# Performance work log

Hardware: AMD Instinct MI355X
Metric: run time of the kernel (lower is better)

The kernel has to match this reference:

```python
import jax, jax.numpy as jnp
import numpy as np

B, S, E = 2, 2048, 4096
H, HKV, D = 32, 8, 128          # num_heads, num_kv_heads, head_dim
ROT = 128                        # rotary_emb_dim (full head)
ROPE_BASE = 10000.0


def setup_inputs() -> dict:
    key = jax.random.key(0)
    ks = jax.random.split(key, 9)
    s = lambda fan_in: 1.0 / np.sqrt(fan_in)
    return {
        "x": jax.random.normal(ks[0], (B, S, E), jnp.float32),
        "wq_w": jax.random.normal(ks[1], (E, E), jnp.float32) * s(E),
        "wq_b": jax.random.normal(ks[2], (E,), jnp.float32) * 0.01,
        "wk_w": jax.random.normal(ks[3], (E, HKV * D), jnp.float32) * s(E),
        "wk_b": jax.random.normal(ks[4], (HKV * D,), jnp.float32) * 0.01,
        "wv_w": jax.random.normal(ks[5], (E, HKV * D), jnp.float32) * s(E),
        "wv_b": jax.random.normal(ks[6], (HKV * D,), jnp.float32) * 0.01,
        "wo_w": jax.random.normal(ks[7], (E, E), jnp.float32) * s(E),
        "wo_b": jax.random.normal(ks[8], (E,), jnp.float32) * 0.01,
    }


def _interleave_to_half(t):
    # torch.cat([t[..., ::2], t[..., 1::2]], dim=-1)
    return jnp.concatenate([t[..., 0::2], t[..., 1::2]], axis=-1)


def _apply_rope(t):
    # non-interleaved (rotate-half) rotary on first ROT dims of head_dim
    half = ROT // 2
    inv_freq = 1.0 / (ROPE_BASE ** (jnp.arange(0, ROT, 2, dtype=jnp.float32) / ROT))
    pos = jnp.arange(t.shape[1], dtype=jnp.float32)
    freqs = pos[:, None] * inv_freq[None, :]            # (S, ROT/2)
    cos = jnp.cos(freqs)[None, :, None, :]              # (1,S,1,ROT/2)
    sin = jnp.sin(freqs)[None, :, None, :]
    t1, t2 = t[..., :half], t[..., half:ROT]
    rot = jnp.concatenate([t1 * cos - t2 * sin, t1 * sin + t2 * cos], axis=-1)
    return jnp.concatenate([rot, t[..., ROT:]], axis=-1)


def reference(x, wq_w, wq_b, wk_w, wk_b, wv_w, wv_b, wo_w, wo_b):
    b, s, _ = x.shape
    q = (x @ wq_w + wq_b).reshape(b, s, H, D)           # bshd
    k = (x @ wk_w + wk_b).reshape(b, s, HKV, D)
    v = (x @ wv_w + wv_b).reshape(b, s, HKV, D)
    # inline even/odd interleave (rot_embed_HF_impl=False path)
    q = _apply_rope(_interleave_to_half(q))
    k = _apply_rope(_interleave_to_half(k))
    # GQA: replicate kv heads
    rep = H // HKV
    k = jnp.repeat(k, rep, axis=2)                      # (b,s,H,D)
    v = jnp.repeat(v, rep, axis=2)
    scale = 1.0 / jnp.sqrt(jnp.asarray(D, x.dtype))
    scores = jnp.einsum("bqhd,bkhd->bhqk", q, k) * scale
    causal = jnp.tril(jnp.ones((s, s), bool))
    scores = jnp.where(causal[None, None], scores, jnp.finfo(x.dtype).min)
    p = jax.nn.softmax(scores, axis=-1)
    ctx = jnp.einsum("bhqk,bkhd->bqhd", p, v).reshape(b, s, E)
    return ctx @ wo_w + wo_b
```

## Files before the change

### kernel.cpp

```cpp
#include <hip/hip_runtime.h>

typedef unsigned short u16;
typedef unsigned int   u32;
typedef __attribute__((ext_vector_type(4))) float f32x4;
typedef __attribute__((ext_vector_type(4))) u32   u32x4;
typedef __attribute__((ext_vector_type(8))) short bf16x8;

#define B_   2
#define S_   2048
#define E_   4096
#define H_   32
#define HKV_ 8
#define D_   128
#define M_   (B_*S_)

__device__ __forceinline__ u16 f2bf(float f) {
  union { float f; u32 u; } v; v.f = f;
  u32 u = v.u;
  return (u16)((u + 0x7fffu + ((u >> 16) & 1u)) >> 16);
}
__device__ __forceinline__ float bf2f(u16 v) {
  union { u32 u; float f; } x; x.u = ((u32)v) << 16; return x.f;
}

__device__ __forceinline__ void gl_lds16(const u16* g, u16* l) {
  __builtin_amdgcn_global_load_lds((const __attribute__((address_space(1))) void*)g,
                                   (__attribute__((address_space(3))) void*)l,
                                   16, 0, 0);
}

__global__ __launch_bounds__(256) void k_cast_bf16(const float* __restrict__ in,
                                                   u16* __restrict__ out, int n8) {
  int i = blockIdx.x * 256 + threadIdx.x;
  if (i >= n8) return;
  const f32x4* p = (const f32x4*)in + (size_t)i * 2;
  f32x4 a = p[0], b = p[1];
  u32x4 r;
  r.x = f2bf(a.x) | ((u32)f2bf(a.y) << 16);
  r.y = f2bf(a.z) | ((u32)f2bf(a.w) << 16);
  r.z = f2bf(b.x) | ((u32)f2bf(b.y) << 16);
  r.w = f2bf(b.z) | ((u32)f2bf(b.w) << 16);
  *((u32x4*)out + i) = r;
}

__global__ __launch_bounds__(256) void k_transpose_cast(const float* __restrict__ W,
                                                        u16* __restrict__ WT,
                                                        int K, int N) {
  __shared__ float tile[32][33];
  int x = threadIdx.x, y = threadIdx.y;
  int n0 = blockIdx.x * 32, k0 = blockIdx.y * 32;
#pragma unroll
  for (int i = 0; i < 32; i += 8)
    tile[y + i][x] = W[(size_t)(k0 + y + i) * N + n0 + x];
  __syncthreads();
#pragma unroll
  for (int i = 0; i < 32; i += 8)
    WT[(size_t)(n0 + y + i) * K + k0 + x] = f2bf(tile[x][y + i]);
}

__global__ __launch_bounds__(256) void k_transpose_v(const u16* __restrict__ V,
                                                     u16* __restrict__ Vt) {
  __shared__ u16 t[32][33];
  int x = threadIdx.x, y = threadIdx.y;
  int d0 = blockIdx.x * 32, s0 = blockIdx.y * 32, z = blockIdx.z;
  int b = z >> 3, hk = z & 7;
#pragma unroll
  for (int i = 0; i < 32; i += 8)
    t[y + i][x] = V[((size_t)(b*S_ + s0 + y + i) * HKV_ + hk) * D_ + d0 + x];
  __syncthreads();
#pragma unroll
  for (int i = 0; i < 32; i += 8)
    Vt[((size_t)(z*D_ + d0 + y + i)) * S_ + s0 + x] = t[x][y + i];
}

__device__ __forceinline__ void storeC(float* C, size_t idx, float v) { C[idx] = v; }
__device__ __forceinline__ void storeC(u16*   C, size_t idx, float v) { C[idx] = f2bf(v); }

template<typename OUTT>
__global__ __launch_bounds__(256, 2) void k_gemm_bt(const u16* __restrict__ A,
                                                    const u16* __restrict__ BT,
                                                    const float* __restrict__ bias,
                                                    OUTT* __restrict__ C,
                                                    int M, int N, int K) {
  __shared__ u16 As[128 * 32];
  __shared__ u16 Bs[128 * 32];
  int tid  = threadIdx.x;
  int wave = tid >> 6, lane = tid & 63;
  int bm = blockIdx.y * 128, bn = blockIdx.x * 128;
  int wm = (wave >> 1) * 64, wn = (wave & 1) * 64;
  int ml = lane & 15, kq = (lane >> 4) * 8;

  int srow = wave * 16 + (lane >> 2);
  int scol = (lane & 3) * 8;
  const u16* Ab0 = A  + (size_t)(bm + srow)      * K + scol;
  const u16* Ab1 = A  + (size_t)(bm + srow + 64) * K + scol;
  const u16* Bb0 = BT + (size_t)(bn + srow)      * K + scol;
  const u16* Bb1 = BT + (size_t)(bn + srow + 64) * K + scol;
  u16* a0 = &As[wave * 512];        u16* a1 = &As[2048 + wave * 512];
  u16* b0 = &Bs[wave * 512];        u16* b1 = &Bs[2048 + wave * 512];

  f32x4 acc[4][4];
#pragma unroll
  for (int i = 0; i < 4; ++i)
#pragma unroll
    for (int j = 0; j < 4; ++j) { f32x4 z = {0.f,0.f,0.f,0.f}; acc[i][j] = z; }

  for (int kt = 0; kt < K; kt += 32) {
    gl_lds16(Ab0 + kt, a0);
    gl_lds16(Ab1 + kt, a1);
    gl_lds16(Bb0 + kt, b0);
    gl_lds16(Bb1 + kt, b1);
    __syncthreads();
    bf16x8 af[4], bfr[4];
#pragma unroll
    for (int i = 0; i < 4; ++i) {
      af[i]  = *(const bf16x8*)&As[(wm + i*16 + ml) * 32 + kq];
      bfr[i] = *(const bf16x8*)&Bs[(wn + i*16 + ml) * 32 + kq];
    }
#pragma unroll
    for (int mi = 0; mi < 4; ++mi)
#pragma unroll
      for (int ni = 0; ni < 4; ++ni)
        acc[mi][ni] = __builtin_amdgcn_mfma_f32_16x16x32_bf16(af[mi], bfr[ni],
                                                              acc[mi][ni], 0, 0, 0);
    __syncthreads();
  }
  int rq = (lane >> 4) * 4;
#pragma unroll
  for (int mi = 0; mi < 4; ++mi)
#pragma unroll
    for (int ni = 0; ni < 4; ++ni) {
      int col = bn + wn + ni*16 + ml;
      float bv = bias[col];
#pragma unroll
      for (int r = 0; r < 4; ++r) {
        int row = bm + wm + mi*16 + rq + r;
        storeC(C, (size_t)row * N + col, acc[mi][ni][r] + bv);
      }
    }
}

__global__ __launch_bounds__(256) void k_rope_bf(u16* __restrict__ T, int nrows, int hshift) {
  int gw   = (blockIdx.x * 256 + threadIdx.x) >> 6;
  int lane = threadIdx.x & 63;
  if (gw >= nrows) return;
  u16* row = T + (size_t)gw * 128;
  float v0 = bf2f(row[2*lane]), v1 = bf2f(row[2*lane + 1]);
  int s = (gw >> hshift) & (S_ - 1);
  float inv = expf((float)lane * -0.14391156831212787f);
  float fr  = (float)s * inv;
  float sn, cs;
  sincosf(fr, &sn, &cs);
  row[lane]      = f2bf(v0 * cs - v1 * sn);
  row[lane + 64] = f2bf(v0 * sn + v1 * cs);
}

#define TQB 128
__global__ __launch_bounds__(256, 2) void k_attn_mfma(const u16* __restrict__ Qb,
                                                      const u16* __restrict__ Kb,
                                                      const u16* __restrict__ Vt,
                                                      u16* __restrict__ ctx) {
  __shared__ u16 Ks[32][136];
  __shared__ u16 Vs[128][40];
  __shared__ u16 Ps[4][32][40];
  int tid = threadIdx.x, wave = tid >> 6, lane = tid & 63;
  int qb = (int)(gridDim.x - 1 - blockIdx.x);
  int h = blockIdx.y, b = blockIdx.z;
  int hk = h >> 2;
  int q0 = qb * TQB + wave * 32;
  int ml = lane & 15, quad = lane >> 4;

  bf16x8 qf[2][4];
#pragma unroll
  for (int g = 0; g < 2; ++g) {
    const u16* qp = Qb + ((size_t)((b*S_ + q0 + g*16 + ml) * H_ + h)) * D_ + quad * 8;
#pragma unroll
    for (int kk = 0; kk < 4; ++kk) qf[g][kk] = *(const bf16x8*)(qp + kk * 32);
  }
  f32x4 of[2][8], lsum[2];
#pragma unroll
  for (int g = 0; g < 2; ++g) {
    f32x4 z = {0.f,0.f,0.f,0.f};
    lsum[g] = z;
#pragma unroll
    for (int i = 0; i < 8; ++i) of[g][i] = z;
  }
  bf16x8 ones;
#pragma unroll
  for (int i = 0; i < 8; ++i) ones[i] = (short)0x3F80;

  int skey = tid >> 3, sdc = (tid & 7) * 16;
  int svd  = tid >> 1, svk = (tid & 1) * 16;
  const u16* kbase = Kb + ((size_t)(b*S_ + skey) * HKV_ + hk) * D_ + sdc;
  const u16* vbase = Vt + ((size_t)(b*HKV_ + hk) * D_ + svd) * S_ + svk;

  const float SCL2E = 0.12751721769649596f;
  int ntiles = 4 * qb + 4;

  u32x4 rk0 = *(const u32x4*)kbase;
  u32x4 rk1 = *(const u32x4*)(kbase + 8);
  u32x4 rv0 = *(const u32x4*)vbase;
  u32x4 rv1 = *(const u32x4*)(vbase + 8);

  for (int kt = 0; kt < ntiles; ++kt) {
    int ks0 = kt * 32;
    __syncthreads();
    *(u32x4*)&Ks[skey][sdc]     = rk0;
    *(u32x4*)&Ks[skey][sdc + 8] = rk1;
    *(u32x4*)&Vs[svd][svk]      = rv0;
    *(u32x4*)&Vs[svd][svk + 8]  = rv1;
    __syncthreads();
    if (kt + 1 < ntiles) {
      size_t ko = (size_t)(ks0 + 32) * (HKV_ * D_);
      rk0 = *(const u32x4*)(kbase + ko);
      rk1 = *(const u32x4*)(kbase + ko + 8);
      rv0 = *(const u32x4*)(vbase + ks0 + 32);
      rv1 = *(const u32x4*)(vbase + ks0 + 40);
    }
    if (ks0 > q0 + 31) continue;

    f32x4 sc[2][2];
    { f32x4 z = {0.f,0.f,0.f,0.f}; sc[0][0]=z; sc[0][1]=z; sc[1][0]=z; sc[1][1]=z; }
    __builtin_amdgcn_s_setprio(1);
#pragma unroll
    for (int kk = 0; kk < 4; ++kk) {
      bf16x8 k0 = *(const bf16x8*)&Ks[ml     ][kk*32 + quad*8];
      bf16x8 k1 = *(const bf16x8*)&Ks[ml + 16][kk*32 + quad*8];
#pragma unroll
      for (int g = 0; g < 2; ++g) {
        sc[g][0] = __builtin_amdgcn_mfma_f32_16x16x32_bf16(qf[g][kk], k0, sc[g][0], 0, 0, 0);
        sc[g][1] = __builtin_amdgcn_mfma_f32_16x16x32_bf16(qf[g][kk], k1, sc[g][1], 0, 0, 0);
      }
    }
    __builtin_amdgcn_s_setprio(0);
#pragma unroll
    for (int g = 0; g < 2; ++g) {
      int qrow = q0 + g*16 + quad * 4;
#pragma unroll
      for (int r = 0; r < 4; ++r) {
        float e0 = (ks0 + ml      <= qrow + r)
                 ? __builtin_amdgcn_exp2f(sc[g][0][r] * SCL2E) : 0.f;
        float e1 = (ks0 + ml + 16 <= qrow + r)
                 ? __builtin_amdgcn_exp2f(sc[g][1][r] * SCL2E) : 0.f;
        Ps[wave][g*16 + quad*4 + r][ml]      = f2bf(e0);
        Ps[wave][g*16 + quad*4 + r][ml + 16] = f2bf(e1);
      }
    }
    bf16x8 pf[2];
    pf[0] = *(const bf16x8*)&Ps[wave][ml     ][quad * 8];
    pf[1] = *(const bf16x8*)&Ps[wave][ml + 16][quad * 8];
    __builtin_amdgcn_s_setprio(1);
    lsum[0] = __builtin_amdgcn_mfma_f32_16x16x32_bf16(pf[0], ones, lsum[0], 0, 0, 0);
    lsum[1] = __builtin_amdgcn_mfma_f32_16x16x32_bf16(pf[1], ones, lsum[1], 0, 0, 0);
#pragma unroll
    for (int nt = 0; nt < 8; ++nt) {
      bf16x8 vf = *(const bf16x8*)&Vs[nt*16 + ml][quad * 8];
      of[0][nt] = __builtin_amdgcn_mfma_f32_16x16x32_bf16(pf[0], vf, of[0][nt], 0, 0, 0);
      of[1][nt] = __builtin_amdgcn_mfma_f32_16x16x32_bf16(pf[1], vf, of[1][nt], 0, 0, 0);
    }
    __builtin_amdgcn_s_setprio(0);
  }
#pragma unroll
  for (int g = 0; g < 2; ++g) {
    u16* cp = ctx + ((size_t)((b*S_ + q0 + g*16 + quad*4) * H_ + h)) * D_ + ml;
#pragma unroll
    for (int r = 0; r < 4; ++r) {
      float inv = 1.0f / lsum[g][r];
#pragma unroll
      for (int nt = 0; nt < 8; ++nt)
        cp[(size_t)r * H_ * D_ + nt*16] = f2bf(of[g][nt][r] * inv);
    }
  }
}

extern "C" void kernel_launch(void* const* d_in, const int* in_sizes, int n_in,
                              void* d_out, int out_size, void* d_ws, size_t ws_size,
                              hipStream_t stream) {
  const float* x    = (const float*)d_in[0];
  const float* wq_w = (const float*)d_in[1];
  const float* wq_b = (const float*)d_in[2];
  const float* wk_w = (const float*)d_in[3];
  const float* wk_b = (const float*)d_in[4];
  const float* wv_w = (const float*)d_in[5];
  const float* wv_b = (const float*)d_in[6];
  const float* wo_w = (const float*)d_in[7];
  const float* wo_b = (const float*)d_in[8];
  float* out = (float*)d_out;

  char* ws = (char*)d_ws;
  size_t off = 0;
  u16* xb  = (u16*)(ws + off); off += (size_t)M_ * E_ * 2;
  u16* wqT = (u16*)(ws + off); off += (size_t)E_ * E_ * 2;
  u16* wkT = (u16*)(ws + off); off += (size_t)E_ * (HKV_*D_) * 2;
  u16* wvT = (u16*)(ws + off); off += (size_t)E_ * (HKV_*D_) * 2;
  u16* woT = (u16*)(ws + off); off += (size_t)E_ * E_ * 2;
  u16* Qb  = (u16*)(ws + off); off += (size_t)M_ * E_ * 2;
  u16* Kb  = (u16*)(ws + off); off += (size_t)M_ * HKV_ * D_ * 2;
  u16* Vb  = (u16*)(ws + off); off += (size_t)M_ * HKV_ * D_ * 2;
  u16* Vt  = (u16*)(ws + off); off += (size_t)M_ * HKV_ * D_ * 2;
  u16* ctxb = xb;

  k_cast_bf16<<<(M_*E_/8)/256, 256, 0, stream>>>(x, xb, M_*E_/8);
  k_transpose_cast<<<dim3(E_/32,        E_/32), dim3(32,8), 0, stream>>>(wq_w, wqT, E_, E_);
  k_transpose_cast<<<dim3((HKV_*D_)/32, E_/32), dim3(32,8), 0, stream>>>(wk_w, wkT, E_, HKV_*D_);
  k_transpose_cast<<<dim3((HKV_*D_)/32, E_/32), dim3(32,8), 0, stream>>>(wv_w, wvT, E_, HKV_*D_);
  k_transpose_cast<<<dim3(E_/32,        E_/32), dim3(32,8), 0, stream>>>(wo_w, woT, E_, E_);

  k_gemm_bt<u16><<<dim3(E_/128,        M_/128), 256, 0, stream>>>(xb, wqT, wq_b, Qb, M_, E_,       E_);
  k_gemm_bt<u16><<<dim3((HKV_*D_)/128, M_/128), 256, 0, stream>>>(xb, wkT, wk_b, Kb, M_, HKV_*D_, E_);
  k_gemm_bt<u16><<<dim3((HKV_*D_)/128, M_/128), 256, 0, stream>>>(xb, wvT, wv_b, Vb, M_, HKV_*D_, E_);

  k_rope_bf<<<(M_*H_)/4,   256, 0, stream>>>(Qb, M_*H_,   5);
  k_rope_bf<<<(M_*HKV_)/4, 256, 0, stream>>>(Kb, M_*HKV_, 3);

  k_transpose_v<<<dim3(D_/32, S_/32, B_*HKV_), dim3(32,8), 0, stream>>>(Vb, Vt);

  k_attn_mfma<<<dim3(S_/TQB, H_, B_), 256, 0, stream>>>(Qb, Kb, Vt, ctxb);

  k_gemm_bt<float><<<dim3(E_/128, M_/128), 256, 0, stream>>>(ctxb, woT, wo_b, out, M_, E_, E_);
}
```

Before: 902.5 us.

## Add 256x256 double-buffered MFMA GEMM for Q and output projections

Introduces a 512-thread GEMM kernel with 256x256 output tiles, double-buffered LDS filled by direct global-to-LDS loads, XOR swizzling, and phased MFMA compute with wave priority boosts. It replaces the 128x128 GEMM for the large Q projection and the output projection. The aim is more data reuse per tile and overlap of the next tile's loads with compute. It uses far more LDS and registers per block, which limits occupancy and leaves only one wave of blocks on the grid.

```diff
diff --git a/kernel.cpp b/kernel.cpp
--- a/kernel.cpp
+++ b/kernel.cpp
@@ -138,6 +138,112 @@
         storeC(C, (size_t)row * N + col, acc[mi][ni][r] + bv);
       }
     }
+}
+
+#define READ_A(MH) \
+  _Pragma("unroll") for (int mm = 0; mm < 4; ++mm) \
+    _Pragma("unroll") for (int kk = 0; kk < 2; ++kk) \
+      af[mm][kk] = *(const bf16x8*)&lds[bufc + (wr*128 + (MH)*64 + mm*16 + ml)*64 + ((kk*32 + c0) ^ swz)];
+#define READ_B(NH, BV) \
+  _Pragma("unroll") for (int nn = 0; nn < 2; ++nn) \
+    _Pragma("unroll") for (int kk = 0; kk < 2; ++kk) \
+      BV[nn][kk] = *(const bf16x8*)&lds[bufc + 16384 + (wc*64 + (NH)*32 + nn*16 + ml)*64 + ((kk*32 + c0) ^ swz)];
+#define PHASE_MFMA(MB, NB, BV) \
+  __builtin_amdgcn_s_setprio(1); \
+  _Pragma("unroll") for (int mm = 0; mm < 4; ++mm) \
+    _Pragma("unroll") for (int nn = 0; nn < 2; ++nn) \
+      _Pragma("unroll") for (int kk = 0; kk < 2; ++kk) \
+        acc[(MB)+mm][(NB)+nn] = __builtin_amdgcn_mfma_f32_16x16x32_bf16( \
+            af[mm][kk], BV[nn][kk], acc[(MB)+mm][(NB)+nn], 0, 0, 0); \
+  __builtin_amdgcn_s_setprio(0);
+
+template<typename OUTT>
+__global__ __launch_bounds__(512, 2) void k_gemm256(const u16* __restrict__ A,
+                                                    const u16* __restrict__ BT,
+                                                    const float* __restrict__ bias,
+                                                    OUTT* __restrict__ C,
+                                                    int M, int N, int K) {
+  __shared__ u16 lds[65536];
+  const int tid = threadIdx.x, wave = tid >> 6, lane = tid & 63;
+  const int wr = wave >> 2, wc = wave & 3;
+  const int ml = lane & 15, quad = lane >> 4;
+  const int swz = (ml & 7) << 3;
+  const int c0 = quad * 8;
+  const int bm = blockIdx.y * 256, bn = blockIdx.x * 256;
+
+  const int srow = tid >> 3;
+  const int scol = 8 * ((tid & 7) ^ (srow & 7));
+  const u16* Ag = A  + (size_t)(bm + srow) * K + scol;
+  const u16* Bg = BT + (size_t)(bn + srow) * K + scol;
+  const int stA = wave * 512;
+  const int stB = 16384 + wave * 512;
+
+  f32x4 acc[8][4];
+#pragma unroll
+  for (int i = 0; i < 8; ++i)
+#pragma unroll
+    for (int j = 0; j < 4; ++j) { f32x4 z = {0.f,0.f,0.f,0.f}; acc[i][j] = z; }
+
+  const int NT = K >> 6;
+#pragma unroll
+  for (int j = 0; j < 4; ++j) gl_lds16(Ag + (size_t)j*64*K, &lds[stA + j*4096]);
+#pragma unroll
+  for (int j = 0; j < 4; ++j) gl_lds16(Bg + (size_t)j*64*K, &lds[stB + j*4096]);
+  asm volatile("s_waitcnt vmcnt(0)");
+  __builtin_amdgcn_sched_barrier(0);
+  __builtin_amdgcn_s_barrier();
+
+  bf16x8 af[4][2], b0[2][2], b1[2][2];
+  for (int t = 0; t < NT; ++t) {
+    const int bufc = (t & 1) << 15;
+    const int bufn = bufc ^ 32768;
+    READ_A(0)
+    READ_B(0, b0)
+    if (t + 1 < NT) {
+      const u16* An = Ag + (size_t)(t + 1) * 64;
+      const u16* Bn = Bg + (size_t)(t + 1) * 64;
+#pragma unroll
+      for (int j = 0; j < 4; ++j) gl_lds16(An + (size_t)j*64*K, &lds[bufn + stA + j*4096]);
+#pragma unroll
+      for (int j = 0; j < 4; ++j) gl_lds16(Bn + (size_t)j*64*K, &lds[bufn + stB + j*4096]);
+    }
+    __builtin_amdgcn_s_barrier();
+    asm volatile("s_waitcnt lgkmcnt(0)");
+    __builtin_amdgcn_sched_barrier(0);
+    PHASE_MFMA(0, 0, b0)
+    __builtin_amdgcn_s_barrier();
+    READ_B(1, b1)
+    __builtin_amdgcn_s_barrier();
+    asm volatile("s_waitcnt lgkmcnt(0)");
+    __builtin_amdgcn_sched_barrier(0);
+    PHASE_MFMA(0, 2, b1)
+    __builtin_amdgcn_s_barrier();
+    READ_A(1)
+    __builtin_amdgcn_s_barrier();
+    asm volatile("s_waitcnt lgkmcnt(0)");
+    __builtin_amdgcn_sched_barrier(0);
+    PHASE_MFMA(4, 0, b0)
+    __builtin_amdgcn_s_barrier();
+    if (t + 1 < NT) {
+      asm volatile("s_waitcnt vmcnt(0)");
+      __builtin_amdgcn_sched_barrier(0);
+    }
+    __builtin_amdgcn_s_barrier();
+    PHASE_MFMA(4, 2, b1)
+    __builtin_amdgcn_s_barrier();
+  }
+#pragma unroll
+  for (int n = 0; n < 4; ++n) {
+    int col = bn + wc*64 + n*16 + ml;
+    float bv = bias[col];
+#pragma unroll
+    for (int m = 0; m < 8; ++m)
+#pragma unroll
+      for (int r = 0; r < 4; ++r) {
+        int row = bm + wr*128 + m*16 + quad*4 + r;
+        storeC(C, (size_t)row * N + col, acc[m][n][r] + bv);
+      }
+  }
 }
 
 __global__ __launch_bounds__(256) void k_rope_bf(u16* __restrict__ T, int nrows, int hshift) {
@@ -306,7 +412,7 @@
   k_transpose_cast<<<dim3((HKV_*D_)/32, E_/32), dim3(32,8), 0, stream>>>(wv_w, wvT, E_, HKV_*D_);
   k_transpose_cast<<<dim3(E_/32,        E_/32), dim3(32,8), 0, stream>>>(wo_w, woT, E_, E_);
 
-  k_gemm_bt<u16><<<dim3(E_/128,        M_/128), 256, 0, stream>>>(xb, wqT, wq_b, Qb, M_, E_,       E_);
+  k_gemm256<u16><<<dim3(E_/256, M_/256), 512, 0, stream>>>(xb, wqT, wq_b, Qb, M_, E_, E_);
   k_gemm_bt<u16><<<dim3((HKV_*D_)/128, M_/128), 256, 0, stream>>>(xb, wkT, wk_b, Kb, M_, HKV_*D_, E_);
   k_gemm_bt<u16><<<dim3((HKV_*D_)/128, M_/128), 256, 0, stream>>>(xb, wvT, wv_b, Vb, M_, HKV_*D_, E_);
 
@@ -317,5 +423,5 @@
 
   k_attn_mfma<<<dim3(S_/TQB, H_, B_), 256, 0, stream>>>(Qb, Kb, Vt, ctxb);
 
-  k_gemm_bt<float><<<dim3(E_/128, M_/128), 256, 0, stream>>>(ctxb, woT, wo_b, out, M_, E_, E_);
-}
+  k_gemm256<float><<<dim3(E_/256, M_/256), 512, 0, stream>>>(ctxb, woT, wo_b, out, M_, E_, E_);
+}
```

Measured after the change: 878.1 us. 1.03x faster.
